# Performance work log

Measured on AMD Instinct MI355X. Metric: run time of the kernel, lower is better.

## Reference

```python
import jax, jax.numpy as jnp
import numpy as np
from jax import lax

NUM_CLASSES = 80
CONF_THRE = 0.01   # testconf in source
NMS_THRE = 0.2     # nmsthresh in source
N = 8400           # YOLOX anchors at 640x640: 80^2+40^2+20^2
IMG = 640.0


def setup_inputs() -> dict:
    key = jax.random.key(0)
    pred = jax.random.uniform(key, (N, 5 + NUM_CLASSES), dtype=jnp.float32)
    # scale cx,cy,w,h to pixel units so boxes are realistic
    pred = pred.at[:, :4].multiply(IMG)
    return {"prediction": pred}


def _pairwise_iou(boxes):
    # boxes: [N,4] in x1,y1,x2,y2
    area = (boxes[:, 2] - boxes[:, 0]) * (boxes[:, 3] - boxes[:, 1])  # [N]
    lt = jnp.maximum(boxes[:, None, :2], boxes[None, :, :2])  # [N,N,2]
    rb = jnp.minimum(boxes[:, None, 2:], boxes[None, :, 2:])  # [N,N,2]
    wh = jnp.clip(rb - lt, 0.0)
    inter = wh[..., 0] * wh[..., 1]
    return inter / (area[:, None] + area[None, :] - inter + 1e-9)


def reference(prediction):
    # ---- box corner decode (cx,cy,w,h -> x1,y1,x2,y2) ----
    cx, cy, w, h = prediction[:, 0], prediction[:, 1], prediction[:, 2], prediction[:, 3]
    boxes = jnp.stack([cx - w / 2, cy - h / 2, cx + w / 2, cy + h / 2], axis=1)

    # ---- per-class max ----
    cls_scores = prediction[:, 5:5 + NUM_CLASSES]
    class_conf = jnp.max(cls_scores, axis=1, keepdims=True)            # [N,1]
    class_pred = jnp.argmax(cls_scores, axis=1).astype(prediction.dtype)[:, None]

    obj = prediction[:, 4]
    valid = obj >= CONF_THRE                                            # conf mask

    # detections = [x1,y1,x2,y2, obj_conf, class_conf, class_pred]  -> [N,7]
    det = jnp.concatenate([boxes, obj[:, None], class_conf, class_pred], axis=1)

    # ---- class-agnostic greedy NMS on obj score (fixed-shape version) ----
    scores = jnp.where(valid, obj, -1.0)
    order = jnp.argsort(-scores)
    det_s = det[order]
    boxes_s = boxes[order]
    valid_s = valid[order]

    iou = _pairwise_iou(boxes_s)  # [N,N] ~282MB, dominant traffic
    idx = jnp.arange(N)

    def step(keep, inp):
        i, row, v = inp
        alive = keep[i] & v                      # only a kept valid box suppresses
        supp = alive & (row > NMS_THRE) & (idx > i)
        return keep & ~supp, None

    keep0 = jnp.ones((N,), dtype=bool)
    keep, _ = lax.scan(step, keep0, (idx, iou, valid_s))
    keep = keep & valid_s

    # suppressed / below-conf rows are zeroed (torch returns a ragged subset;
    # here we return the score-sorted, mask-zeroed fixed-shape equivalent)
    out = det_s * keep[:, None].astype(det_s.dtype)
    return out
```

## Files before the change

kernel.cpp:

```cpp
#include <hip/hip_runtime.h>
#include <stdint.h>

#define N_BOX 8400
#define NCLS 80
#define PSTRIDE 85
#define NW 132
#define NPAIR 66
#define NTILE 8778
#define ZROWI N_BOX
#define CONF_T 0.01f
#define NMS_T 0.2f

typedef unsigned long long u64;

#define OFF_DET     0
#define OFF_DIAGT   0
#define OFF_SUP1    67584
#define OFF_SUP2    135168
#define OFF_SUP3    202752
#define OFF_KEYS    268800
#define OFF_DETS    336000
#define OFF_BOXESS  604800
#define OFF_MASK    739200
#define OFF_VCNT    9611712
#define OFF_SUP4    9611728
#define OFF_SUP5    9679312

__device__ __forceinline__ unsigned fmap_desc(float f) {
    unsigned u = __float_as_uint(f);
    unsigned m = (u & 0x80000000u) ? ~u : (u | 0x80000000u);
    return ~m;
}

__device__ __forceinline__ u64 readlane64(u64 v, int lane) {
    unsigned lo = (unsigned)__builtin_amdgcn_readlane((int)(unsigned)v, lane);
    unsigned hi = (unsigned)__builtin_amdgcn_readlane((int)(unsigned)(v >> 32), lane);
    return ((u64)hi << 32) | lo;
}

__device__ __forceinline__ u64 shfl_xor64(u64 v, int m) {
    int lo = __shfl_xor((int)(unsigned)v, m);
    int hi = __shfl_xor((int)(unsigned)(v >> 32), m);
    return ((u64)(unsigned)hi << 32) | (unsigned)lo;
}

__device__ __forceinline__ u64 bittranspose64(u64 x, int lane) {
    const u64 P0 = 0x5555555555555555ull, P1 = 0x3333333333333333ull,
              P2 = 0x0F0F0F0F0F0F0F0Full, P3 = 0x00FF00FF00FF00FFull,
              P4 = 0x0000FFFF0000FFFFull, P5 = 0x00000000FFFFFFFFull;
#define TSTEP(s, p) do {                                                 \
        u64 y = shfl_xor64(x, s);                                        \
        x = (lane & (s)) ? ((x & ~(p)) | ((y & ~(p)) >> (s)))            \
                         : ((x & (p))  | ((y & (p))  << (s)));           \
    } while (0)
    TSTEP(1, P0); TSTEP(2, P1); TSTEP(4, P2);
    TSTEP(8, P3); TSTEP(16, P4); TSTEP(32, P5);
#undef TSTEP
    return x;
}

__device__ __forceinline__ u64 wmask(int w, int V) {
    int nb = V - (w << 6);
    if (nb <= 0) return 0ull;
    if (nb >= 64) return ~0ull;
    return (1ull << nb) - 1ull;
}

__device__ __forceinline__ void step_barrier() {
    asm volatile("s_waitcnt lgkmcnt(0)" ::: "memory");
    __builtin_amdgcn_s_barrier();
    asm volatile("" ::: "memory");
}

__global__ __launch_bounds__(256) void prep_k(const float* __restrict__ pred,
                                              float* __restrict__ det,
                                              u64* __restrict__ keys,
                                              u64* __restrict__ mask) {
    if (blockIdx.x == 0 && threadIdx.x < NW)
        mask[(size_t)ZROWI * NW + threadIdx.x] = 0ull;
    int gt = blockIdx.x * 256 + threadIdx.x;
    int i = gt >> 2, q = gt & 3;
    if (i >= N_BOX) return;
    const float* p = pred + (size_t)i * PSTRIDE;
    int cbase = q * 20;
    float best = p[5 + cbase];
    int arg = cbase;
    for (int c = 1; c < 20; ++c) {
        float v = p[5 + cbase + c];
        if (v > best) { best = v; arg = cbase + c; }
    }
    for (int d = 1; d < 4; d <<= 1) {
        float ob = __shfl_xor(best, d);
        int   oa = __shfl_xor(arg, d);
        if (ob > best || (ob == best && oa < arg)) { best = ob; arg = oa; }
    }
    if (q == 0) {
        float cx = p[0], cy = p[1], w = p[2], h = p[3], obj = p[4];
        float hw = __fmul_rn(w, 0.5f), hh = __fmul_rn(h, 0.5f);
        float x1 = __fsub_rn(cx, hw), y1 = __fsub_rn(cy, hh);
        float x2 = __fadd_rn(cx, hw), y2 = __fadd_rn(cy, hh);
        bool valid = (obj >= CONF_T);
        float score = valid ? obj : -1.0f;
        keys[i] = ((u64)fmap_desc(score) << 32) | (unsigned)i;
        float4* dr = (float4*)(det + (size_t)i * 8);
        dr[0] = make_float4(x1, y1, x2, y2);
        dr[1] = make_float4(obj, best, (float)arg, 0.0f);
    }
}

__global__ __launch_bounds__(256) void rank_k(const u64* __restrict__ keys,
                                              const float* __restrict__ det,
                                              float4* __restrict__ det_s,
                                              float4* __restrict__ boxes_s,
                                              int* __restrict__ vcount) {
    int t = threadIdx.x;
    int i = blockIdx.x * 32 + (t & 31);
    int s = t >> 5;
    u64 my = (i < N_BOX) ? keys[i] : ~0ull;
    int cnt = 0, cv = 0;
    int j0 = s * 1050, j1 = j0 + 1050;
    for (int j = j0; j < j1; j += 2) {
        ulonglong2 kk = *(const ulonglong2*)(keys + j);
        cnt += (kk.x < my) + (kk.y < my);
        cv  += ((long long)kk.x >= 0) + ((long long)kk.y >= 0);
    }
    __shared__ int sc[256], sv[256];
    sc[t] = cnt; sv[t] = cv;
    __syncthreads();
    if (t < 32) {
        int r = sc[t] + sc[t + 32] + sc[t + 64] + sc[t + 96]
              + sc[t + 128] + sc[t + 160] + sc[t + 192] + sc[t + 224];
        if (i < N_BOX) {
            const float4* dr = (const float4*)(det + (size_t)i * 8);
            float4 b0 = dr[0], b1 = dr[1];
            det_s[(size_t)r * 2]     = b0;
            det_s[(size_t)r * 2 + 1] = b1;
            boxes_s[r] = b0;
        }
        if (blockIdx.x == 0 && t == 0) {
            *vcount = sv[0] + sv[32] + sv[64] + sv[96]
                    + sv[128] + sv[160] + sv[192] + sv[224];
        }
    }
}

__global__ __launch_bounds__(256) void mask_k(const float4* __restrict__ boxes_s,
                                              u64* __restrict__ mask,
                                              u64* __restrict__ diagT,
                                              u64* __restrict__ sup1,
                                              u64* __restrict__ sup2,
                                              u64* __restrict__ sup3,
                                              u64* __restrict__ sup4,
                                              u64* __restrict__ sup5) {
    int sub = threadIdx.x >> 6, lane = threadIdx.x & 63;
    int tt = blockIdx.x * 4 + sub;
    bool tv = (tt < NTILE);
    __shared__ float4 cB[4][64];
    __shared__ float  cA[4][64];
    int rb = 0, cb = 0;
    if (tv) {
        rb = (int)((2.0f * NW + 1.0f
                    - sqrtf((2.0f * NW + 1.0f) * (2.0f * NW + 1.0f) - 8.0f * (float)tt)) * 0.5f);
        while (rb > 0 && rb * NW - rb * (rb - 1) / 2 > tt) rb--;
        while ((rb + 1) * NW - (rb + 1) * rb / 2 <= tt) rb++;
        cb = rb + (tt - (rb * NW - rb * (rb - 1) / 2));
        int c0 = cb * 64 + lane;
        float4 b = (c0 < N_BOX) ? boxes_s[c0] : make_float4(0.f, 0.f, 0.f, 0.f);
        cB[sub][lane] = b;
        cA[sub][lane] = __fmul_rn(__fsub_rn(b.z, b.x), __fsub_rn(b.w, b.y));
    }
    __syncthreads();
    if (!tv) return;
    int r = rb * 64 + lane;
    bool inb = (r < N_BOX);
    float4 rx = boxes_s[inb ? r : (N_BOX - 1)];
    float ra = __fmul_rn(__fsub_rn(rx.z, rx.x), __fsub_rn(rx.w, rx.y));
    u64 bits = 0ull;
    int cbase = cb * 64;
    for (int j = 0; j < 64; ++j) {
        int c = cbase + j;
        if (c >= N_BOX || c <= r) continue;
        float4 cx4 = cB[sub][j];
        float ltx = fmaxf(rx.x, cx4.x), lty = fmaxf(rx.y, cx4.y);
        float rbx = fminf(rx.z, cx4.z), rby = fminf(rx.w, cx4.w);
        float wx = fmaxf(__fsub_rn(rbx, ltx), 0.0f);
        float wy = fmaxf(__fsub_rn(rby, lty), 0.0f);
        float inter = __fmul_rn(wx, wy);
        float denom = __fadd_rn(__fsub_rn(__fadd_rn(ra, cA[sub][j]), inter), 1e-9f);
        float iou = __fdiv_rn(inter, denom);
        if (iou > NMS_T) bits |= (1ull << j);
    }
    if (inb) mask[(size_t)r * NW + cb] = bits;
    int d = cb - rb;
    if (d <= 5) {
        u64 tb = bittranspose64(bits, lane);
        size_t idx = (size_t)cb * 64 + lane;
        if (d == 0)      diagT[idx] = tb;
        else if (d == 1) sup1[idx]  = tb;
        else if (d == 2) sup2[idx]  = tb;
        else if (d == 3) sup3[idx]  = tb;
        else if (d == 4) sup4[idx]  = tb;
        else             sup5[idx]  = tb;
    }
}

__global__ __launch_bounds__(256, 1) void scan_k(const u64* __restrict__ mask,
                                                 const u64* __restrict__ diagT,
                                                 const u64* __restrict__ sup1,
                                                 const u64* __restrict__ sup2,
                                                 const u64* __restrict__ sup3,
                                                 const u64* __restrict__ sup4,
                                                 const u64* __restrict__ sup5,
                                                 const int* __restrict__ vcount,
                                                 const float* __restrict__ det_s,
                                                 float* __restrict__ out) {
    __shared__ u64 remvP1[NW + 4];
    __shared__ u64 remvP2[NW + 4];
    __shared__ u64 Lbuf[NW];
    int tid = threadIdx.x, lane = tid & 63, wv = tid >> 6;
    int V = *vcount;
    for (int i = tid; i < NW + 4; i += 256) { remvP1[i] = 0ull; remvP2[i] = 0ull; }
    for (int i = tid; i < NW; i += 256) Lbuf[i] = 0ull;
    __syncthreads();

    if (wv == 0) {
        u64 A1 = 0ull, A2 = 0ull, A3 = 0ull, A4 = 0ull;
        u64 dEP,s1EP,s2EP,s3EP,s4EP, dOP,s1OP,s2OP,s3OP,s4OP,s5OP;
        u64 dEQ,s1EQ,s2EQ,s3EQ,s4EQ, dOQ,s1OQ,s2OQ,s3OQ,s4OQ,s5OQ;
#define TL(S, pp) do {                                                   \
        int p_ = (pp) < NPAIR ? (pp) : (NPAIR - 1);                      \
        size_t ex_ = (size_t)(2 * p_) * 64 + lane;                       \
        size_t ox_ = ex_ + 64;                                           \
        dE##S = diagT[ex_]; s1E##S = sup1[ex_]; s2E##S = sup2[ex_];      \
        s3E##S = sup3[ex_]; s4E##S = sup4[ex_];                          \
        dO##S = diagT[ox_]; s1O##S = sup1[ox_]; s2O##S = sup2[ox_];      \
        s3O##S = sup3[ox_]; s4O##S = sup4[ox_]; s5O##S = sup5[ox_];      \
    } while (0)
#define RES(curv, dd, mm, Lout) do {                                     \
        u64 ns_ = (~(curv)) & (mm);                                      \
        Lout = 0ull;                                                     \
        while (ns_) {                                                    \
            int b_ = __builtin_ctzll(ns_);                               \
            Lout |= 1ull << b_;                                          \
            u64 sup_ = __ballot((int)((dd >> b_) & 1ull));               \
            ns_ &= ~sup_;                                                \
            ns_ &= ~(1ull << b_);                                        \
        }                                                                \
    } while (0)
#define STEP0(tt_, S) do {                                               \
        int e_ = 2 * (tt_), o_ = e_ + 1;                                 \
        u64 cur_ = remvP1[e_] | remvP2[e_];                              \
        cur_ |= __ballot((s1E##S & A1) != 0ull);                         \
        cur_ |= __ballot((s2E##S & A2) != 0ull);                         \
        cur_ |= __ballot((s3E##S & A3) != 0ull);                         \
        cur_ |= __ballot((s4E##S & A4) != 0ull);                         \
        u64 Le_;                                                         \
        RES(cur_, dE##S, wmask(e_, V), Le_);                             \
        u64 curo_ = remvP1[o_] | remvP2[o_];                             \
        curo_ |= __ballot((s1O##S & Le_) != 0ull);                       \
        curo_ |= __ballot((s2O##S & A1) != 0ull);                        \
        curo_ |= __ballot((s3O##S & A2) != 0ull);                        \
        curo_ |= __ballot((s4O##S & A3) != 0ull);                        \
        curo_ |= __ballot((s5O##S & A4) != 0ull);                        \
        u64 Lo_;                                                         \
        RES(curo_, dO##S, wmask(o_, V), Lo_);                            \
        if (lane == 0) { Lbuf[e_] = Le_; Lbuf[o_] = Lo_; }               \
        A4 = A2; A3 = A1; A2 = Le_; A1 = Lo_;                            \
        TL(S, (tt_) + 2);                                                \
        step_barrier();                                                  \
    } while (0)
        TL(P, 0);
        TL(Q, 1);
        for (int t = 0; t < NPAIR; t += 2) {
            STEP0(t, P);
            STEP0(t + 1, Q);
        }
#undef STEP0
#undef RES
#undef TL
    } else if (wv <= 2) {
        int half = wv - 1;
        u64* myP = half ? remvP2 : remvP1;
        int tw = (lane < 4) ? (128 + lane) : 131;
        u64 Ra = 0ull, Rb = 0ull, Rc = 0ull;
        u64 Pa0=0,Pa1=0,Pa2=0,Pa3=0,Pa4=0,Pa5=0,Pa6=0,Pa7=0;
        u64 Pb0=0,Pb1=0,Pb2=0,Pb3=0,Pb4=0,Pb5=0,Pb6=0,Pb7=0;
        u64 Pc0=0,Pc1=0,Pc2=0,Pc3=0,Pc4=0,Pc5=0,Pc6=0,Pc7=0;
        u64 Qa0=0,Qa1=0,Qa2=0,Qa3=0,Qa4=0,Qa5=0,Qa6=0,Qa7=0;
        u64 Qb0=0,Qb1=0,Qb2=0,Qb3=0,Qb4=0,Qb5=0,Qb6=0,Qb7=0;
        u64 Qc0=0,Qc1=0,Qc2=0,Qc3=0,Qc4=0,Qc5=0,Qc6=0,Qc7=0;

#define CONS(S) do {                                                     \
        Ra |= ((S##a0|S##a1)|(S##a2|S##a3))|((S##a4|S##a5)|(S##a6|S##a7));\
        Rb |= ((S##b0|S##b1)|(S##b2|S##b3))|((S##b4|S##b5)|(S##b6|S##b7));\
        Rc |= ((S##c0|S##c1)|(S##c2|S##c3))|((S##c4|S##c5)|(S##c6|S##c7));\
    } while (0)

#define PUB(w_) do {                                                     \
        u64 rw_ = ((w_) < 128) ? (((w_) & 1) ? Rb : Ra) : Rc;            \
        int sl_ = ((w_) < 128) ? ((w_) >> 1) : ((w_) - 128);             \
        u64 pv_ = readlane64(rw_, sl_);                                  \
        if (lane == 0) myP[w_] = pv_;                                    \
    } while (0)

#define LROW(S, i, remv_, rbase_) do {                                   \
        size_t ri_ = (remv_) ? (size_t)((rbase_) + __builtin_ctz(remv_)) \
                             : (size_t)ZROWI;                            \
        (remv_) &= (remv_) - 1u;                                         \
        const u64* rp_ = mask + ri_ * NW;                                \
        ulonglong2 v_ = *(const ulonglong2*)(rp_ + 2 * lane);            \
        S##a##i = v_.x; S##b##i = v_.y; S##c##i = rp_[tw];               \
    } while (0)

#define XTRA(remv_, rbase_) do {                                         \
        while (remv_) {                                                  \
            u64 xa_ = 0, xb_ = 0, xc_ = 0;                               \
            for (int q_ = 0; q_ < 8; ++q_) {                             \
                size_t ri_ = (remv_) ? (size_t)((rbase_) + __builtin_ctz(remv_)) \
                                     : (size_t)ZROWI;                    \
                (remv_) &= (remv_) - 1u;                                 \
                const u64* rp_ = mask + ri_ * NW;                        \
                ulonglong2 v_ = *(const ulonglong2*)(rp_ + 2 * lane);    \
                xa_ |= v_.x; xb_ |= v_.y; xc_ |= rp_[tw];                \
            }                                                            \
            Ra |= xa_; Rb |= xb_; Rc |= xc_;                             \
        }                                                                \
    } while (0)

#define STEP1(tt_, Siss, Scon) do {                                      \
        int t_ = (tt_);                                                  \
        CONS(Scon);                       \
        PUB(2 * t_ + 2);                                                 \
        PUB(2 * t_ + 3);                                                 \
        u64 Le_ = (t_ >= 1) ? Lbuf[2 * t_ - 2] : 0ull;                   \
        u64 Lo_ = (t_ >= 1) ? Lbuf[2 * t_ - 1] : 0ull;                   \
        unsigned re_ = half ? (unsigned)(Le_ >> 32) : (unsigned)Le_;     \
        unsigned ro_ = half ? (unsigned)(Lo_ >> 32) : (unsigned)Lo_;     \
        int rbe_ = ((2 * t_ - 2) << 6) + 32 * half;                      \
        int rbo_ = rbe_ + 64;                                            \
        LROW(Siss, 0, re_, rbe_); LROW(Siss, 1, re_, rbe_);              \
        LROW(Siss, 2, re_, rbe_); LROW(Siss, 3, re_, rbe_);              \
        LROW(Siss, 4, ro_, rbo_); LROW(Siss, 5, ro_, rbo_);              \
        LROW(Siss, 6, ro_, rbo_); LROW(Siss, 7, ro_, rbo_);              \
        XTRA(re_, rbe_);                                                 \
        XTRA(ro_, rbo_);                                                 \
        step_barrier();                                                  \
    } while (0)

        for (int t = 0; t < NPAIR; t += 2) {
            STEP1(t, P, Q);
            STEP1(t + 1, Q, P);
        }
#undef STEP1
#undef XTRA
#undef LROW
#undef PUB
#undef CONS
    } else {
        for (int t = 0; t < NPAIR; ++t) {
            if (t >= 1) {
                int r0 = (2 * t - 2) * 64 + lane;
                int r1 = r0 + 64;
                bool k0 = (Lbuf[2 * t - 2] >> lane) & 1ull;
                bool k1 = (Lbuf[2 * t - 1] >> lane) & 1ull;
                const float4* d0 = (const float4*)(det_s + (size_t)r0 * 8);
                const float4* d1 = (const float4*)(det_s + (size_t)r1 * 8);
                float4 a0 = d0[0], a1 = d0[1], b0 = d1[0], b1 = d1[1];
                float* o0 = out + (size_t)r0 * 7;
                float* o1 = out + (size_t)r1 * 7;
                o0[0]=k0?a0.x:0.f; o0[1]=k0?a0.y:0.f; o0[2]=k0?a0.z:0.f;
                o0[3]=k0?a0.w:0.f; o0[4]=k0?a1.x:0.f; o0[5]=k0?a1.y:0.f;
                o0[6]=k0?a1.z:0.f;
                o1[0]=k1?b0.x:0.f; o1[1]=k1?b0.y:0.f; o1[2]=k1?b0.z:0.f;
                o1[3]=k1?b0.w:0.f; o1[4]=k1?b1.x:0.f; o1[5]=k1?b1.y:0.f;
                o1[6]=k1?b1.z:0.f;
            }
            step_barrier();
        }
    }

    __syncthreads();
    for (int r = 8320 + tid; r < N_BOX; r += 256) {
        bool k = (Lbuf[r >> 6] >> (r & 63)) & 1ull;
        const float4* dr = (const float4*)(det_s + (size_t)r * 8);
        float4 b0 = dr[0], b1 = dr[1];
        float* op = out + (size_t)r * 7;
        op[0] = k ? b0.x : 0.0f;
        op[1] = k ? b0.y : 0.0f;
        op[2] = k ? b0.z : 0.0f;
        op[3] = k ? b0.w : 0.0f;
        op[4] = k ? b1.x : 0.0f;
        op[5] = k ? b1.y : 0.0f;
        op[6] = k ? b1.z : 0.0f;
    }
}

extern "C" void kernel_launch(void* const* d_in, const int* in_sizes, int n_in,
                              void* d_out, int out_size, void* d_ws, size_t ws_size,
                              hipStream_t stream) {
    const float* pred = (const float*)d_in[0];
    char* ws = (char*)d_ws;
    float*    det     = (float*)   (ws + OFF_DET);
    u64*      diagT   = (u64*)     (ws + OFF_DIAGT);
    u64*      sup1    = (u64*)     (ws + OFF_SUP1);
    u64*      sup2    = (u64*)     (ws + OFF_SUP2);
    u64*      sup3    = (u64*)     (ws + OFF_SUP3);
    u64*      sup4    = (u64*)     (ws + OFF_SUP4);
    u64*      sup5    = (u64*)     (ws + OFF_SUP5);
    u64*      keys    = (u64*)     (ws + OFF_KEYS);
    float*    det_s   = (float*)   (ws + OFF_DETS);
    float4*   boxes_s = (float4*)  (ws + OFF_BOXESS);
    u64*      mask    = (u64*)     (ws + OFF_MASK);
    int*      vcount  = (int*)     (ws + OFF_VCNT);

    prep_k<<<132, 256, 0, stream>>>(pred, det, keys, mask);
    rank_k<<<264, 256, 0, stream>>>(keys, det, (float4*)det_s, boxes_s, vcount);
    mask_k<<<(NTILE + 3) / 4, 256, 0, stream>>>(boxes_s, mask, diagT, sup1, sup2,
                                                sup3, sup4, sup5);
    scan_k<<<1, 256, 0, stream>>>(mask, diagT, sup1, sup2, sup3, sup4, sup5,
                                  vcount, det_s, (float*)d_out);
}
```

Baseline: 138.6 us.

## Fuse four NMS stages into one persistent kernel with grid barriers

```diff
diff --git a/kernel.cpp b/kernel.cpp
--- a/kernel.cpp
+++ b/kernel.cpp
@@ -7,9 +7,11 @@
 #define NW 132
 #define NPAIR 66
 #define NTILE 8778
+#define NGRP 2195
 #define ZROWI N_BOX
 #define CONF_T 0.01f
 #define NMS_T 0.2f
+#define GRIDB 512
 
 typedef unsigned long long u64;
 
@@ -25,6 +27,7 @@
 #define OFF_VCNT    9611712
 #define OFF_SUP4    9611728
 #define OFF_SUP5    9679312
+#define OFF_GBAR    9746896
 
 __device__ __forceinline__ unsigned fmap_desc(float f) {
     unsigned u = __float_as_uint(f);
@@ -72,152 +75,172 @@
     asm volatile("" ::: "memory");
 }
 
-__global__ __launch_bounds__(256) void prep_k(const float* __restrict__ pred,
-                                              float* __restrict__ det,
-                                              u64* __restrict__ keys,
-                                              u64* __restrict__ mask) {
-    if (blockIdx.x == 0 && threadIdx.x < NW)
-        mask[(size_t)ZROWI * NW + threadIdx.x] = 0ull;
-    int gt = blockIdx.x * 256 + threadIdx.x;
-    int i = gt >> 2, q = gt & 3;
-    if (i >= N_BOX) return;
-    const float* p = pred + (size_t)i * PSTRIDE;
-    int cbase = q * 20;
-    float best = p[5 + cbase];
-    int arg = cbase;
-    for (int c = 1; c < 20; ++c) {
-        float v = p[5 + cbase + c];
-        if (v > best) { best = v; arg = cbase + c; }
-    }
-    for (int d = 1; d < 4; d <<= 1) {
-        float ob = __shfl_xor(best, d);
-        int   oa = __shfl_xor(arg, d);
-        if (ob > best || (ob == best && oa < arg)) { best = ob; arg = oa; }
-    }
-    if (q == 0) {
-        float cx = p[0], cy = p[1], w = p[2], h = p[3], obj = p[4];
-        float hw = __fmul_rn(w, 0.5f), hh = __fmul_rn(h, 0.5f);
-        float x1 = __fsub_rn(cx, hw), y1 = __fsub_rn(cy, hh);
-        float x2 = __fadd_rn(cx, hw), y2 = __fadd_rn(cy, hh);
-        bool valid = (obj >= CONF_T);
-        float score = valid ? obj : -1.0f;
-        keys[i] = ((u64)fmap_desc(score) << 32) | (unsigned)i;
-        float4* dr = (float4*)(det + (size_t)i * 8);
-        dr[0] = make_float4(x1, y1, x2, y2);
-        dr[1] = make_float4(obj, best, (float)arg, 0.0f);
-    }
-}
-
-__global__ __launch_bounds__(256) void rank_k(const u64* __restrict__ keys,
-                                              const float* __restrict__ det,
-                                              float4* __restrict__ det_s,
-                                              float4* __restrict__ boxes_s,
-                                              int* __restrict__ vcount) {
-    int t = threadIdx.x;
-    int i = blockIdx.x * 32 + (t & 31);
-    int s = t >> 5;
-    u64 my = (i < N_BOX) ? keys[i] : ~0ull;
-    int cnt = 0, cv = 0;
-    int j0 = s * 1050, j1 = j0 + 1050;
-    for (int j = j0; j < j1; j += 2) {
-        ulonglong2 kk = *(const ulonglong2*)(keys + j);
-        cnt += (kk.x < my) + (kk.y < my);
-        cv  += ((long long)kk.x >= 0) + ((long long)kk.y >= 0);
-    }
-    __shared__ int sc[256], sv[256];
-    sc[t] = cnt; sv[t] = cv;
+__device__ __forceinline__ void gbar(int* c, int nb, bool spin) {
     __syncthreads();
-    if (t < 32) {
-        int r = sc[t] + sc[t + 32] + sc[t + 64] + sc[t + 96]
-              + sc[t + 128] + sc[t + 160] + sc[t + 192] + sc[t + 224];
-        if (i < N_BOX) {
-            const float4* dr = (const float4*)(det + (size_t)i * 8);
-            float4 b0 = dr[0], b1 = dr[1];
-            det_s[(size_t)r * 2]     = b0;
-            det_s[(size_t)r * 2 + 1] = b1;
-            boxes_s[r] = b0;
-        }
-        if (blockIdx.x == 0 && t == 0) {
-            *vcount = sv[0] + sv[32] + sv[64] + sv[96]
-                    + sv[128] + sv[160] + sv[192] + sv[224];
-        }
-    }
-}
-
-__global__ __launch_bounds__(256) void mask_k(const float4* __restrict__ boxes_s,
-                                              u64* __restrict__ mask,
-                                              u64* __restrict__ diagT,
-                                              u64* __restrict__ sup1,
-                                              u64* __restrict__ sup2,
-                                              u64* __restrict__ sup3,
-                                              u64* __restrict__ sup4,
-                                              u64* __restrict__ sup5) {
-    int sub = threadIdx.x >> 6, lane = threadIdx.x & 63;
-    int tt = blockIdx.x * 4 + sub;
-    bool tv = (tt < NTILE);
+    if (threadIdx.x == 0) {
+        __threadfence();
+        atomicAdd(c, 1);
+        if (spin) {
+            while (__hip_atomic_load(c, __ATOMIC_ACQUIRE,
+                                     __HIP_MEMORY_SCOPE_AGENT) < nb)
+                __builtin_amdgcn_s_sleep(2);
+        }
+        __threadfence();
+    }
+    __syncthreads();
+}
+
+__global__ __launch_bounds__(256, 4) void fused_k(const float* __restrict__ pred,
+                                                  char* __restrict__ ws,
+                                                  float* __restrict__ out) {
+    float*  det     = (float*) (ws + OFF_DET);
+    u64*    diagT   = (u64*)   (ws + OFF_DIAGT);
+    u64*    sup1    = (u64*)   (ws + OFF_SUP1);
+    u64*    sup2    = (u64*)   (ws + OFF_SUP2);
+    u64*    sup3    = (u64*)   (ws + OFF_SUP3);
+    u64*    sup4    = (u64*)   (ws + OFF_SUP4);
+    u64*    sup5    = (u64*)   (ws + OFF_SUP5);
+    u64*    keys    = (u64*)   (ws + OFF_KEYS);
+    float*  det_s   = (float*) (ws + OFF_DETS);
+    float4* boxes_s = (float4*)(ws + OFF_BOXESS);
+    u64*    mask    = (u64*)   (ws + OFF_MASK);
+    int*    vcount  = (int*)   (ws + OFF_VCNT);
+    int*    gb      = (int*)   (ws + OFF_GBAR);
+
     __shared__ float4 cB[4][64];
     __shared__ float  cA[4][64];
-    int rb = 0, cb = 0;
-    if (tv) {
-        rb = (int)((2.0f * NW + 1.0f
-                    - sqrtf((2.0f * NW + 1.0f) * (2.0f * NW + 1.0f) - 8.0f * (float)tt)) * 0.5f);
-        while (rb > 0 && rb * NW - rb * (rb - 1) / 2 > tt) rb--;
-        while ((rb + 1) * NW - (rb + 1) * rb / 2 <= tt) rb++;
-        cb = rb + (tt - (rb * NW - rb * (rb - 1) / 2));
-        int c0 = cb * 64 + lane;
-        float4 b = (c0 < N_BOX) ? boxes_s[c0] : make_float4(0.f, 0.f, 0.f, 0.f);
-        cB[sub][lane] = b;
-        cA[sub][lane] = __fmul_rn(__fsub_rn(b.z, b.x), __fsub_rn(b.w, b.y));
-    }
-    __syncthreads();
-    if (!tv) return;
-    int r = rb * 64 + lane;
-    bool inb = (r < N_BOX);
-    float4 rx = boxes_s[inb ? r : (N_BOX - 1)];
-    float ra = __fmul_rn(__fsub_rn(rx.z, rx.x), __fsub_rn(rx.w, rx.y));
-    u64 bits = 0ull;
-    int cbase = cb * 64;
-    for (int j = 0; j < 64; ++j) {
-        int c = cbase + j;
-        if (c >= N_BOX || c <= r) continue;
-        float4 cx4 = cB[sub][j];
-        float ltx = fmaxf(rx.x, cx4.x), lty = fmaxf(rx.y, cx4.y);
-        float rbx = fminf(rx.z, cx4.z), rby = fminf(rx.w, cx4.w);
-        float wx = fmaxf(__fsub_rn(rbx, ltx), 0.0f);
-        float wy = fmaxf(__fsub_rn(rby, lty), 0.0f);
-        float inter = __fmul_rn(wx, wy);
-        float denom = __fadd_rn(__fsub_rn(__fadd_rn(ra, cA[sub][j]), inter), 1e-9f);
-        float iou = __fdiv_rn(inter, denom);
-        if (iou > NMS_T) bits |= (1ull << j);
-    }
-    if (inb) mask[(size_t)r * NW + cb] = bits;
-    int d = cb - rb;
-    if (d <= 5) {
-        u64 tb = bittranspose64(bits, lane);
-        size_t idx = (size_t)cb * 64 + lane;
-        if (d == 0)      diagT[idx] = tb;
-        else if (d == 1) sup1[idx]  = tb;
-        else if (d == 2) sup2[idx]  = tb;
-        else if (d == 3) sup3[idx]  = tb;
-        else if (d == 4) sup4[idx]  = tb;
-        else             sup5[idx]  = tb;
-    }
-}
-
-__global__ __launch_bounds__(256, 1) void scan_k(const u64* __restrict__ mask,
-                                                 const u64* __restrict__ diagT,
-                                                 const u64* __restrict__ sup1,
-                                                 const u64* __restrict__ sup2,
-                                                 const u64* __restrict__ sup3,
-                                                 const u64* __restrict__ sup4,
-                                                 const u64* __restrict__ sup5,
-                                                 const int* __restrict__ vcount,
-                                                 const float* __restrict__ det_s,
-                                                 float* __restrict__ out) {
+    __shared__ int    sc[256], sv[256];
     __shared__ u64 remvP1[NW + 4];
     __shared__ u64 remvP2[NW + 4];
     __shared__ u64 Lbuf[NW];
-    int tid = threadIdx.x, lane = tid & 63, wv = tid >> 6;
+
+    int tid = threadIdx.x;
+    int bid = blockIdx.x;
+
+    for (int b = bid; b < 132; b += GRIDB) {
+        if (b == 0 && tid < NW) mask[(size_t)ZROWI * NW + tid] = 0ull;
+        int gt = b * 256 + tid;
+        int i = gt >> 2, q = gt & 3;
+        if (i < N_BOX) {
+            const float* p = pred + (size_t)i * PSTRIDE;
+            int cbase = q * 20;
+            float best = p[5 + cbase];
+            int arg = cbase;
+            for (int c = 1; c < 20; ++c) {
+                float v = p[5 + cbase + c];
+                if (v > best) { best = v; arg = cbase + c; }
+            }
+            for (int d = 1; d < 4; d <<= 1) {
+                float ob = __shfl_xor(best, d);
+                int   oa = __shfl_xor(arg, d);
+                if (ob > best || (ob == best && oa < arg)) { best = ob; arg = oa; }
+            }
+            if (q == 0) {
+                float cx = p[0], cy = p[1], w = p[2], h = p[3], obj = p[4];
+                float hw = __fmul_rn(w, 0.5f), hh = __fmul_rn(h, 0.5f);
+                float x1 = __fsub_rn(cx, hw), y1 = __fsub_rn(cy, hh);
+                float x2 = __fadd_rn(cx, hw), y2 = __fadd_rn(cy, hh);
+                bool valid = (obj >= CONF_T);
+                float score = valid ? obj : -1.0f;
+                keys[i] = ((u64)fmap_desc(score) << 32) | (unsigned)i;
+                float4* dr = (float4*)(det + (size_t)i * 8);
+                dr[0] = make_float4(x1, y1, x2, y2);
+                dr[1] = make_float4(obj, best, (float)arg, 0.0f);
+            }
+        }
+    }
+    gbar(gb + 0, GRIDB, true);
+
+    for (int b = bid; b < 264; b += GRIDB) {
+        int i = b * 32 + (tid & 31);
+        int s = tid >> 5;
+        u64 my = (i < N_BOX) ? keys[i] : ~0ull;
+        int cnt = 0, cv = 0;
+        int j0 = s * 1050, j1 = j0 + 1050;
+        for (int j = j0; j < j1; j += 2) {
+            ulonglong2 kk = *(const ulonglong2*)(keys + j);
+            cnt += (kk.x < my) + (kk.y < my);
+            cv  += ((long long)kk.x >= 0) + ((long long)kk.y >= 0);
+        }
+        sc[tid] = cnt; sv[tid] = cv;
+        __syncthreads();
+        if (tid < 32) {
+            int r = sc[tid] + sc[tid + 32] + sc[tid + 64] + sc[tid + 96]
+                  + sc[tid + 128] + sc[tid + 160] + sc[tid + 192] + sc[tid + 224];
+            if (i < N_BOX) {
+                const float4* dr = (const float4*)(det + (size_t)i * 8);
+                float4 b0 = dr[0], b1 = dr[1];
+                float4* ds4 = (float4*)det_s;
+                ds4[(size_t)r * 2]     = b0;
+                ds4[(size_t)r * 2 + 1] = b1;
+                boxes_s[r] = b0;
+            }
+            if (b == 0 && tid == 0) {
+                *vcount = sv[0] + sv[32] + sv[64] + sv[96]
+                        + sv[128] + sv[160] + sv[192] + sv[224];
+            }
+        }
+        __syncthreads();
+    }
+    gbar(gb + 1, GRIDB, true);
+
+    for (int g = bid; g < NGRP; g += GRIDB) {
+        __syncthreads();
+        int sub = tid >> 6, lane = tid & 63;
+        int tt = g * 4 + sub;
+        bool tv = (tt < NTILE);
+        int rb = 0, cb = 0;
+        if (tv) {
+            rb = (int)((2.0f * NW + 1.0f
+                        - sqrtf((2.0f * NW + 1.0f) * (2.0f * NW + 1.0f) - 8.0f * (float)tt)) * 0.5f);
+            while (rb > 0 && rb * NW - rb * (rb - 1) / 2 > tt) rb--;
+            while ((rb + 1) * NW - (rb + 1) * rb / 2 <= tt) rb++;
+            cb = rb + (tt - (rb * NW - rb * (rb - 1) / 2));
+            int c0 = cb * 64 + lane;
+            float4 b = (c0 < N_BOX) ? boxes_s[c0] : make_float4(0.f, 0.f, 0.f, 0.f);
+            cB[sub][lane] = b;
+            cA[sub][lane] = __fmul_rn(__fsub_rn(b.z, b.x), __fsub_rn(b.w, b.y));
+        }
+        __syncthreads();
+        if (tv) {
+            int r = rb * 64 + lane;
+            bool inb = (r < N_BOX);
+            float4 rx = boxes_s[inb ? r : (N_BOX - 1)];
+            float ra = __fmul_rn(__fsub_rn(rx.z, rx.x), __fsub_rn(rx.w, rx.y));
+            u64 bits = 0ull;
+            int cbase = cb * 64;
+            for (int j = 0; j < 64; ++j) {
+                int c = cbase + j;
+                if (c >= N_BOX || c <= r) continue;
+                float4 cx4 = cB[sub][j];
+                float ltx = fmaxf(rx.x, cx4.x), lty = fmaxf(rx.y, cx4.y);
+                float rbx = fminf(rx.z, cx4.z), rby = fminf(rx.w, cx4.w);
+                float wx = fmaxf(__fsub_rn(rbx, ltx), 0.0f);
+                float wy = fmaxf(__fsub_rn(rby, lty), 0.0f);
+                float inter = __fmul_rn(wx, wy);
+                float denom = __fadd_rn(__fsub_rn(__fadd_rn(ra, cA[sub][j]), inter), 1e-9f);
+                float iou = __fdiv_rn(inter, denom);
+                if (iou > NMS_T) bits |= (1ull << j);
+            }
+            if (inb) mask[(size_t)r * NW + cb] = bits;
+            int d = cb - rb;
+            if (d <= 5) {
+                u64 tb = bittranspose64(bits, lane);
+                size_t idx = (size_t)cb * 64 + lane;
+                if (d == 0)      diagT[idx] = tb;
+                else if (d == 1) sup1[idx]  = tb;
+                else if (d == 2) sup2[idx]  = tb;
+                else if (d == 3) sup3[idx]  = tb;
+                else if (d == 4) sup4[idx]  = tb;
+                else             sup5[idx]  = tb;
+            }
+        }
+    }
+    gbar(gb + 2, GRIDB, bid == 0);
+
+    if (bid != 0) return;
+
+    int lane = tid & 63, wv = tid >> 6;
     int V = *vcount;
     for (int i = tid; i < NW + 4; i += 256) { remvP1[i] = 0ull; remvP2[i] = 0ull; }
     for (int i = tid; i < NW; i += 256) Lbuf[i] = 0ull;
@@ -400,23 +423,6 @@
                               hipStream_t stream) {
     const float* pred = (const float*)d_in[0];
     char* ws = (char*)d_ws;
-    float*    det     = (float*)   (ws + OFF_DET);
-    u64*      diagT   = (u64*)     (ws + OFF_DIAGT);
-    u64*      sup1    = (u64*)     (ws + OFF_SUP1);
-    u64*      sup2    = (u64*)     (ws + OFF_SUP2);
-    u64*      sup3    = (u64*)     (ws + OFF_SUP3);
-    u64*      sup4    = (u64*)     (ws + OFF_SUP4);
-    u64*      sup5    = (u64*)     (ws + OFF_SUP5);
-    u64*      keys    = (u64*)     (ws + OFF_KEYS);
-    float*    det_s   = (float*)   (ws + OFF_DETS);
-    float4*   boxes_s = (float4*)  (ws + OFF_BOXESS);
-    u64*      mask    = (u64*)     (ws + OFF_MASK);
-    int*      vcount  = (int*)     (ws + OFF_VCNT);
-
-    prep_k<<<132, 256, 0, stream>>>(pred, det, keys, mask);
-    rank_k<<<264, 256, 0, stream>>>(keys, det, (float4*)det_s, boxes_s, vcount);
-    mask_k<<<(NTILE + 3) / 4, 256, 0, stream>>>(boxes_s, mask, diagT, sup1, sup2,
-                                                sup3, sup4, sup5);
-    scan_k<<<1, 256, 0, stream>>>(mask, diagT, sup1, sup2, sup3, sup4, sup5,
-                                  vcount, det_s, (float*)d_out);
-}
+    hipMemsetAsync(ws + OFF_GBAR, 0, 3 * sizeof(int), stream);
+    fused_k<<<GRIDB, 256, 0, stream>>>(pred, ws, (float*)d_out);
+}
```

Result: slower. 385.5 us (+178.1%).
